# Optimization experiments

Hardware: AMD Instinct MI355X
Metric: run time of the kernel (lower is better)

## Reference

```python
import jax, jax.numpy as jnp
import numpy as np

# GlobalAttention block from GATESynergy: to_dense_batch -> multi-head
# masked self-attention per graph -> scatter back to sparse + residual.
B, NMAX, DIN, DOUT, H = 512, 160, 128, 128, 4
DH = DOUT // H  # 32
COUNTS = np.where(np.arange(B) % 2 == 0, 96, 160)  # nodes per graph, sum=65536
T = int(COUNTS.sum())


def _xavier(key, dout, din):
    lim = np.sqrt(6.0 / (din + dout)).astype(np.float32)
    return jax.random.uniform(key, (dout, din), jnp.float32, -lim, lim)


def setup_inputs() -> dict:
    key = jax.random.key(0)
    ks = jax.random.split(key, 5)
    batch = jnp.asarray(np.repeat(np.arange(B), COUNTS), dtype=jnp.int32)
    x = jax.random.normal(ks[0], (T, DIN), jnp.float32)
    return {
        "x": x,
        "batch": batch,
        "Wq": _xavier(ks[1], DOUT, DIN), "bq": jnp.zeros((DOUT,), jnp.float32),
        "Wk": _xavier(ks[2], DOUT, DIN), "bk": jnp.zeros((DOUT,), jnp.float32),
        "Wv": _xavier(ks[3], DOUT, DIN), "bv": jnp.zeros((DOUT,), jnp.float32),
        "Wo": _xavier(ks[4], DOUT, DOUT), "bo": jnp.zeros((DOUT,), jnp.float32),
    }


def reference(x, batch, Wq, bq, Wk, bk, Wv, bv, Wo, bo):
    n = x.shape[0]
    # --- to_dense_batch: sparse [T, D] -> dense [B, NMAX, D] + mask ---
    counts = jax.ops.segment_sum(jnp.ones(n, jnp.int32), batch, num_segments=B)
    starts = jnp.cumsum(counts) - counts            # first node index per graph
    pos = jnp.arange(n, dtype=jnp.int32) - starts[batch]  # slot within graph
    x_dense = jnp.zeros((B, NMAX, DIN), x.dtype).at[batch, pos].set(x)
    mask = jnp.zeros((B, NMAX), bool).at[batch, pos].set(True)

    def proj(W, b):  # [B,N,DIN] -> [B,H,N,DH]
        return (x_dense @ W.T + b).reshape(B, NMAX, H, DH).transpose(0, 2, 1, 3)

    q, k, v = proj(Wq, bq), proj(Wk, bk), proj(Wv, bv)
    scores = jnp.einsum('bhnd,bhmd->bhnm', q, k) / jnp.sqrt(jnp.asarray(DH, x.dtype))
    scores = jnp.where(mask[:, None, None, :], scores, -jnp.inf)  # mask keys
    attn = jax.nn.softmax(scores, axis=-1)  # dropout p=0.0 -> identity
    out = jnp.einsum('bhnm,bhmd->bnhd', attn, v).reshape(B, NMAX, DOUT)
    out = out @ Wo.T + bo
    out_sparse = out[batch, pos]  # gather valid nodes back to sparse layout
    return out_sparse + x  # residual: in_channels == out_channels
```

## Files before the change

### kernel.cpp

```cpp
#include <hip/hip_runtime.h>

typedef unsigned short u16;
typedef unsigned int u32;
typedef __attribute__((ext_vector_type(8))) short bf16x8;
typedef __attribute__((ext_vector_type(4))) float f32x4;

__device__ __forceinline__ u16 f2bf(float f) {
  u32 u = __builtin_bit_cast(u32, f);
  u += 0x7fffu + ((u >> 16) & 1u);
  return (u16)(u >> 16);
}
__device__ __forceinline__ short f2bs(float f) { return (short)f2bf(f); }

__device__ __forceinline__ bf16x8 cvt8(const float* p) {
  f32x4 a = *reinterpret_cast<const f32x4*>(p);
  f32x4 b = *reinterpret_cast<const f32x4*>(p + 4);
  bf16x8 r;
  r[0] = f2bs(a[0]); r[1] = f2bs(a[1]); r[2] = f2bs(a[2]); r[3] = f2bs(a[3]);
  r[4] = f2bs(b[0]); r[5] = f2bs(b[1]); r[6] = f2bs(b[2]); r[7] = f2bs(b[3]);
  return r;
}
__device__ __forceinline__ bf16x8 lds8(const u16* p) {
  return *reinterpret_cast<const bf16x8*>(p);
}

#define MFMA(a, b, c) __builtin_amdgcn_mfma_f32_16x16x32_bf16((a), (b), (c), 0, 0, 0)

constexpr int DIN = 128, DOUT = 128, DH = 32;
constexpr int T = 65536;
constexpr size_t WFOFF = 0;
constexpr size_t QOFF = 65536;
constexpr size_t KOFF = QOFF + (size_t)4 * T * DH;
constexpr size_t VOFF = KOFF + (size_t)4 * T * DH;
constexpr size_t WS_NEED = (VOFF + (size_t)4 * T * DH) * 2;

__device__ __forceinline__ size_t fragoff(int mat, int ft, int ks) {
  return ((size_t)((mat * 8 + ft) * 4 + ks)) << 9;
}

__global__ void cvtw_kernel(const float* __restrict__ Wq, const float* __restrict__ Wk,
                            const float* __restrict__ Wv, const float* __restrict__ Wo,
                            u16* __restrict__ wf) {
  const int fl = blockIdx.x * 256 + threadIdx.x;
  const int lane = fl & 63, ks = (fl >> 6) & 3, ft = (fl >> 8) & 7, mat = fl >> 11;
  const float* src = mat == 0 ? Wq : mat == 1 ? Wk : mat == 2 ? Wv : Wo;
  const int lr = lane & 15, lg = lane >> 4;
  bf16x8 r = cvt8(src + (ft * 16 + lr) * DIN + ks * 32 + lg * 8);
  *reinterpret_cast<bf16x8*>(wf + (size_t)fl * 8) = r;
}

__global__ __launch_bounds__(256, 2) void qkv_kernel(const float* __restrict__ x,
                                                     const float* __restrict__ bq,
                                                     const float* __restrict__ bk,
                                                     const float* __restrict__ bv,
                                                     u16* __restrict__ ws) {
  const int tid = threadIdx.x;
  const int w = tid >> 6, lane = tid & 63, lg = lane >> 4, lr = lane & 15;
  const size_t rbase = (size_t)blockIdx.x * 128 + w * 32;
  const f32x4 zero = {0.f, 0.f, 0.f, 0.f};
  const u16* wf = ws + WFOFF;
  u16* Q = ws + QOFF;
  u16* K = ws + KOFF;
  u16* V = ws + VOFF;

  bf16x8 xa[2][4];
#pragma unroll
  for (int rt = 0; rt < 2; ++rt)
#pragma unroll
    for (int ks = 0; ks < 4; ++ks)
      xa[rt][ks] = cvt8(x + (rbase + rt * 16 + lr) * DIN + ks * 32 + lg * 8);

#pragma unroll
  for (int ft = 0; ft < 8; ++ft) {
    const int h = ft >> 1, dt = ft & 1;
    bf16x8 wqf[4], wkf[4], wvf[4];
#pragma unroll
    for (int ks = 0; ks < 4; ++ks) {
      wqf[ks] = lds8(wf + fragoff(0, ft, ks) + lane * 8);
      wkf[ks] = lds8(wf + fragoff(1, ft, ks) + lane * 8);
      wvf[ks] = lds8(wf + fragoff(2, ft, ks) + lane * 8);
    }
    f32x4 qacc[2], kacc[2], vacc[2];
#pragma unroll
    for (int rt = 0; rt < 2; ++rt) qacc[rt] = kacc[rt] = vacc[rt] = zero;
#pragma unroll
    for (int rt = 0; rt < 2; ++rt)
#pragma unroll
      for (int ks = 0; ks < 4; ++ks) {
        qacc[rt] = MFMA(xa[rt][ks], wqf[ks], qacc[rt]);
        kacc[rt] = MFMA(xa[rt][ks], wkf[ks], kacc[rt]);
        vacc[rt] = MFMA(wvf[ks], xa[rt][ks], vacc[rt]);
      }
    const float bqv = bq[ft * 16 + lr], bkv = bk[ft * 16 + lr];
    float bvj[4];
#pragma unroll
    for (int j = 0; j < 4; ++j) bvj[j] = bv[ft * 16 + lg * 4 + j];
#pragma unroll
    for (int rt = 0; rt < 2; ++rt) {
      const size_t row0 = rbase + rt * 16;
      const size_t qk_base = (size_t)h * T * DH + (row0 + lg * 4) * DH + dt * 16 + lr;
      const size_t v_base = (size_t)h * T * DH + (((rbase >> 5) + (rt >> 1)) << 10) +
                            (size_t)(dt * 16 + lg * 4) * 32 + (rt & 1) * 16 + lr;
#pragma unroll
      for (int j = 0; j < 4; ++j) {
        Q[qk_base + (size_t)j * DH] = f2bf(qacc[rt][j] + bqv);
        K[qk_base + (size_t)j * DH] = f2bf(kacc[rt][j] + bkv);
        V[v_base + (size_t)j * 32] = f2bf(vacc[rt][j] + bvj[j]);
      }
    }
  }
}

template <int C>
__device__ void attn_wave(const u16* __restrict__ Qh, const u16* __restrict__ Kh,
                          const u16* __restrict__ Vh, int start, int h, int rt,
                          u16 (&strip)[16][168], u16 (&otile)[16][136]) {
  constexpr int NT = C / 16, KB = C / 32;
  const int lane = threadIdx.x & 63, lg = lane >> 4, lr = lane & 15;
  const f32x4 zero = {0.f, 0.f, 0.f, 0.f};
  const int gr = start + rt * 16;

  bf16x8 vb[KB][2];
#pragma unroll
  for (int ks = 0; ks < KB; ++ks)
#pragma unroll
    for (int dt = 0; dt < 2; ++dt)
      vb[ks][dt] = lds8(Vh + (((size_t)(start >> 5) + ks) << 10) +
                        (size_t)(dt * 16 + lr) * 32 + lg * 8);

  const bf16x8 qa = lds8(Qh + (size_t)(gr + lr) * DH + lg * 8);
  f32x4 sacc[NT];
#pragma unroll
  for (int ct = 0; ct < NT; ++ct)
    sacc[ct] = MFMA(qa, lds8(Kh + (size_t)(start + ct * 16 + lr) * DH + lg * 8), zero);

  const float scale = 0.17677669529663687f;
  float m[4], s[4];
#pragma unroll
  for (int j = 0; j < 4; ++j) {
    m[j] = sacc[0][j];
#pragma unroll
    for (int ct = 1; ct < NT; ++ct) m[j] = fmaxf(m[j], sacc[ct][j]);
  }
#pragma unroll
  for (int d = 1; d < 16; d <<= 1) {
#pragma unroll
    for (int j = 0; j < 4; ++j) m[j] = fmaxf(m[j], __shfl_xor(m[j], d, 64));
  }
#pragma unroll
  for (int j = 0; j < 4; ++j) {
    s[j] = 0.f;
#pragma unroll
    for (int ct = 0; ct < NT; ++ct) {
      const float p = __expf((sacc[ct][j] - m[j]) * scale);
      sacc[ct][j] = p;
      s[j] += p;
    }
  }
#pragma unroll
  for (int d = 1; d < 16; d <<= 1) {
#pragma unroll
    for (int j = 0; j < 4; ++j) s[j] += __shfl_xor(s[j], d, 64);
  }
#pragma unroll
  for (int j = 0; j < 4; ++j) {
    const float inv = 1.0f / s[j];
#pragma unroll
    for (int ct = 0; ct < NT; ++ct)
      strip[lg * 4 + j][ct * 16 + lr] = f2bf(sacc[ct][j] * inv);
  }
  asm volatile("s_waitcnt lgkmcnt(0)" ::: "memory");

  f32x4 o0 = zero, o1 = zero;
#pragma unroll
  for (int ks = 0; ks < KB; ++ks) {
    const bf16x8 pa = lds8(&strip[lr][ks * 32 + lg * 8]);
    o0 = MFMA(pa, vb[ks][0], o0);
    o1 = MFMA(pa, vb[ks][1], o1);
  }
#pragma unroll
  for (int j = 0; j < 4; ++j) {
    otile[lg * 4 + j][h * 32 + lr] = f2bf(o0[j]);
    otile[lg * 4 + j][h * 32 + 16 + lr] = f2bf(o1[j]);
  }
}

__global__ __launch_bounds__(256, 3) void attn_kernel(const u16* __restrict__ ws,
                                                      const float* __restrict__ bo,
                                                      const float* __restrict__ x,
                                                      float* __restrict__ out) {
  __shared__ u16 strip[4][16][168];
  __shared__ u16 otile[16][136];
  const int w = threadIdx.x >> 6, lane = threadIdx.x & 63;
  const int lg = lane >> 4, lr = lane & 15;
  const int phys = blockIdx.x;
  const int xcd = phys & 7, idx = phys >> 3;
  const int t = idx & 15;
  const int p = (idx >> 4) * 8 + xcd;
  const int h = w;
  const u16* Qh = ws + QOFF + (size_t)h * T * DH;
  const u16* Kh = ws + KOFF + (size_t)h * T * DH;
  const u16* Vh = ws + VOFF + (size_t)h * T * DH;

  int gr;
  if (t < 6) {
    attn_wave<96>(Qh, Kh, Vh, p * 256, h, t, strip[w], otile);
    gr = p * 256 + t * 16;
  } else {
    attn_wave<160>(Qh, Kh, Vh, p * 256 + 96, h, t - 6, strip[w], otile);
    gr = p * 256 + 96 + (t - 6) * 16;
  }
  __syncthreads();

  const u16* wf = ws + WFOFF;
  const f32x4 zero = {0.f, 0.f, 0.f, 0.f};
  bf16x8 oa[4];
#pragma unroll
  for (int ks = 0; ks < 4; ++ks) oa[ks] = lds8(&otile[lr][ks * 32 + lg * 8]);
  f32x4 acc0 = zero, acc1 = zero;
#pragma unroll
  for (int ks = 0; ks < 4; ++ks) {
    acc0 = MFMA(oa[ks], lds8(wf + fragoff(3, w * 2, ks) + lane * 8), acc0);
    acc1 = MFMA(oa[ks], lds8(wf + fragoff(3, w * 2 + 1, ks) + lane * 8), acc1);
  }
  const int c0 = w * 32 + lr, c1 = w * 32 + 16 + lr;
  const float b0 = bo[c0], b1 = bo[c1];
#pragma unroll
  for (int j = 0; j < 4; ++j) {
    const size_t n = (size_t)gr + lg * 4 + j;
    out[n * DOUT + c0] = acc0[j] + b0 + x[n * DIN + c0];
    out[n * DOUT + c1] = acc1[j] + b1 + x[n * DIN + c1];
  }
}

struct SLds1 {
  u16 k[160][40];
  u16 vt[32][168];
  u16 strip[4][16][168];
};

template <int C>
__device__ void attn1(const float* __restrict__ xg, const float* __restrict__ Wq,
                      const float* __restrict__ bq, const float* __restrict__ Wk,
                      const float* __restrict__ bk, const float* __restrict__ Wv,
                      const float* __restrict__ bv, float* __restrict__ og, int h, SLds1& sm) {
  constexpr int NT = C / 16, KB = C / 32, SLOTS = (NT + 3) / 4;
  const int tid = threadIdx.x;
  const int w = tid >> 6, lane = tid & 63, lg = lane >> 4, lr = lane & 15;
  const f32x4 zero = {0.f, 0.f, 0.f, 0.f};

  for (int t = w; t < 2 * NT; t += 4) {
    const int rt = t >> 1, dt = t & 1;
    f32x4 kacc = zero, vacc = zero;
#pragma unroll
    for (int ks = 0; ks < 4; ++ks) {
      bf16x8 xa = cvt8(xg + (rt * 16 + lr) * DIN + ks * 32 + lg * 8);
      bf16x8 wk = cvt8(Wk + (h * DH + dt * 16 + lr) * DIN + ks * 32 + lg * 8);
      bf16x8 wv = cvt8(Wv + (h * DH + dt * 16 + lr) * DIN + ks * 32 + lg * 8);
      kacc = MFMA(xa, wk, kacc);
      vacc = MFMA(wv, xa, vacc);
    }
    const float kb_ = bk[h * DH + dt * 16 + lr];
#pragma unroll
    for (int j = 0; j < 4; ++j) {
      sm.k[rt * 16 + lg * 4 + j][dt * 16 + lr] = f2bf(kacc[j] + kb_);
      sm.vt[dt * 16 + lg * 4 + j][rt * 16 + lr] = f2bf(vacc[j] + bv[h * DH + dt * 16 + lg * 4 + j]);
    }
  }
  __syncthreads();

#pragma unroll
  for (int sl = 0; sl < SLOTS; ++sl) {
    const int rt = w + sl * 4;
    if (rt < NT) {
#pragma unroll
      for (int dt = 0; dt < 2; ++dt) {
        f32x4 qacc = zero;
#pragma unroll
        for (int ks = 0; ks < 4; ++ks) {
          bf16x8 xa = cvt8(xg + (rt * 16 + lr) * DIN + ks * 32 + lg * 8);
          bf16x8 wq = cvt8(Wq + (h * DH + dt * 16 + lr) * DIN + ks * 32 + lg * 8);
          qacc = MFMA(xa, wq, qacc);
        }
        const float bias = bq[h * DH + dt * 16 + lr];
#pragma unroll
        for (int j = 0; j < 4; ++j)
          sm.strip[w][lg * 4 + j][dt * 16 + lr] = f2bf(qacc[j] + bias);
      }
      asm volatile("s_waitcnt lgkmcnt(0)" ::: "memory");
      const bf16x8 qa = lds8(&sm.strip[w][lr][lg * 8]);
      f32x4 sacc[NT];
#pragma unroll
      for (int ct = 0; ct < NT; ++ct)
        sacc[ct] = MFMA(qa, lds8(&sm.k[ct * 16 + lr][lg * 8]), zero);
      const float scale = 0.17677669529663687f;
      float m[4], s[4];
#pragma unroll
      for (int j = 0; j < 4; ++j) {
        m[j] = sacc[0][j];
#pragma unroll
        for (int ct = 1; ct < NT; ++ct) m[j] = fmaxf(m[j], sacc[ct][j]);
      }
#pragma unroll
      for (int d = 1; d < 16; d <<= 1)
#pragma unroll
        for (int j = 0; j < 4; ++j) m[j] = fmaxf(m[j], __shfl_xor(m[j], d, 64));
#pragma unroll
      for (int j = 0; j < 4; ++j) {
        s[j] = 0.f;
#pragma unroll
        for (int ct = 0; ct < NT; ++ct) {
          const float p = __expf((sacc[ct][j] - m[j]) * scale);
          sacc[ct][j] = p;
          s[j] += p;
        }
      }
#pragma unroll
      for (int d = 1; d < 16; d <<= 1)
#pragma unroll
        for (int j = 0; j < 4; ++j) s[j] += __shfl_xor(s[j], d, 64);
#pragma unroll
      for (int j = 0; j < 4; ++j) {
        const float inv = 1.0f / s[j];
#pragma unroll
        for (int ct = 0; ct < NT; ++ct)
          sm.strip[w][lg * 4 + j][ct * 16 + lr] = f2bf(sacc[ct][j] * inv);
      }
      asm volatile("s_waitcnt lgkmcnt(0)" ::: "memory");
      f32x4 o0 = zero, o1 = zero;
#pragma unroll
      for (int ks = 0; ks < KB; ++ks) {
        const bf16x8 pa = lds8(&sm.strip[w][lr][ks * 32 + lg * 8]);
        o0 = MFMA(pa, lds8(&sm.vt[lr][ks * 32 + lg * 8]), o0);
        o1 = MFMA(pa, lds8(&sm.vt[16 + lr][ks * 32 + lg * 8]), o1);
      }
#pragma unroll
      for (int j = 0; j < 4; ++j) {
        const int n = rt * 16 + lg * 4 + j;
        og[n * DOUT + h * DH + lr] = o0[j];
        og[n * DOUT + h * DH + 16 + lr] = o1[j];
      }
    }
  }
}

__global__ __launch_bounds__(256, 3) void fb_k1(const float* __restrict__ x,
                                                const float* __restrict__ Wq,
                                                const float* __restrict__ bq,
                                                const float* __restrict__ Wk,
                                                const float* __restrict__ bk,
                                                const float* __restrict__ Wv,
                                                const float* __restrict__ bv,
                                                float* __restrict__ O) {
  __shared__ SLds1 sm;
  const int bid = blockIdx.x;
  const int g = bid >> 2, h = bid & 3;
  const int p = g >> 1;
  if (g & 1)
    attn1<160>(x + (size_t)(p * 256 + 96) * DIN, Wq, bq, Wk, bk, Wv, bv,
               O + (size_t)(p * 256 + 96) * DOUT, h, sm);
  else
    attn1<96>(x + (size_t)(p * 256) * DIN, Wq, bq, Wk, bk, Wv, bv, O + (size_t)(p * 256) * DOUT,
              h, sm);
}

__global__ __launch_bounds__(256, 4) void fb_k2(float* __restrict__ io, const float* __restrict__ x,
                                                const float* __restrict__ Wo,
                                                const float* __restrict__ bo) {
  const int tid = threadIdx.x;
  const int w = tid >> 6, lane = tid & 63, lg = lane >> 4, lr = lane & 15;
  const f32x4 zero = {0.f, 0.f, 0.f, 0.f};
  const int rbase = blockIdx.x * 128 + w * 32;
  bf16x8 oa[2][4];
#pragma unroll
  for (int r = 0; r < 2; ++r)
#pragma unroll
    for (int ks = 0; ks < 4; ++ks)
      oa[r][ks] = cvt8(io + (size_t)(rbase + r * 16 + lr) * DOUT + ks * 32 + lg * 8);
  f32x4 acc[2][8];
#pragma unroll
  for (int r = 0; r < 2; ++r)
#pragma unroll
    for (int jt = 0; jt < 8; ++jt) acc[r][jt] = zero;
#pragma unroll
  for (int jt = 0; jt < 8; ++jt)
#pragma unroll
    for (int ks = 0; ks < 4; ++ks) {
      const bf16x8 wb = cvt8(Wo + (size_t)(jt * 16 + lr) * DOUT + ks * 32 + lg * 8);
      acc[0][jt] = MFMA(oa[0][ks], wb, acc[0][jt]);
      acc[1][jt] = MFMA(oa[1][ks], wb, acc[1][jt]);
    }
#pragma unroll
  for (int r = 0; r < 2; ++r)
#pragma unroll
    for (int jt = 0; jt < 8; ++jt) {
      const int c = jt * 16 + lr;
      const float bias = bo[c];
#pragma unroll
      for (int j = 0; j < 4; ++j) {
        const size_t n = (size_t)rbase + r * 16 + lg * 4 + j;
        io[n * DOUT + c] = acc[r][jt][j] + bias + x[n * DIN + c];
      }
    }
}

extern "C" void kernel_launch(void* const* d_in, const int* in_sizes, int n_in,
                              void* d_out, int out_size, void* d_ws, size_t ws_size,
                              hipStream_t stream) {
  const float* x = (const float*)d_in[0];
  const float* Wq = (const float*)d_in[2];
  const float* bq = (const float*)d_in[3];
  const float* Wk = (const float*)d_in[4];
  const float* bk = (const float*)d_in[5];
  const float* Wv = (const float*)d_in[6];
  const float* bv = (const float*)d_in[7];
  const float* Wo = (const float*)d_in[8];
  const float* bo = (const float*)d_in[9];
  float* out = (float*)d_out;

  if (ws_size >= WS_NEED) {
    u16* ws = (u16*)d_ws;
    cvtw_kernel<<<dim3(32), dim3(256), 0, stream>>>(Wq, Wk, Wv, Wo, ws);
    qkv_kernel<<<dim3(512), dim3(256), 0, stream>>>(x, bq, bk, bv, ws);
    attn_kernel<<<dim3(4096), dim3(256), 0, stream>>>(ws, bo, x, out);
  } else {
    fb_k1<<<dim3(2048), dim3(256), 0, stream>>>(x, Wq, bq, Wk, bk, Wv, bv, out);
    fb_k2<<<dim3(512), dim3(256), 0, stream>>>(out, x, Wo, bo);
  }
}
```

Baseline: 59.16 us.

## Process two query row tiles per wave, reusing K/V fragments and halving grid

Each attention block now handles two 16-row query tiles instead of one. K fragments are loaded once into registers and shared across both tiles, V fragments are reused likewise, and the grid is halved. The residual x values are prefetched before the barrier so those loads overlap the sync. This cuts redundant K/V global loads and per-block overhead, but raises register pressure and reduces parallelism (fewer blocks).

```diff
diff --git a/kernel.cpp b/kernel.cpp
--- a/kernel.cpp
+++ b/kernel.cpp
@@ -112,13 +112,15 @@
 }
 
 template <int C>
-__device__ void attn_wave(const u16* __restrict__ Qh, const u16* __restrict__ Kh,
-                          const u16* __restrict__ Vh, int start, int h, int rt,
-                          u16 (&strip)[16][168], u16 (&otile)[16][136]) {
+__device__ void attn_wave2(const u16* __restrict__ Qh, const u16* __restrict__ Kh,
+                           const u16* __restrict__ Vh, const u16* __restrict__ wf,
+                           const float* __restrict__ bo, const float* __restrict__ x,
+                           float* __restrict__ out, int start, int h, int t0,
+                           u16 (&strip)[16][168], u16 (&otile)[2][16][136]) {
   constexpr int NT = C / 16, KB = C / 32;
   const int lane = threadIdx.x & 63, lg = lane >> 4, lr = lane & 15;
   const f32x4 zero = {0.f, 0.f, 0.f, 0.f};
-  const int gr = start + rt * 16;
+  const int w = h;
 
   bf16x8 vb[KB][2];
 #pragma unroll
@@ -127,61 +129,103 @@
     for (int dt = 0; dt < 2; ++dt)
       vb[ks][dt] = lds8(Vh + (((size_t)(start >> 5) + ks) << 10) +
                         (size_t)(dt * 16 + lr) * 32 + lg * 8);
-
-  const bf16x8 qa = lds8(Qh + (size_t)(gr + lr) * DH + lg * 8);
-  f32x4 sacc[NT];
+  bf16x8 kf[NT];
 #pragma unroll
   for (int ct = 0; ct < NT; ++ct)
-    sacc[ct] = MFMA(qa, lds8(Kh + (size_t)(start + ct * 16 + lr) * DH + lg * 8), zero);
-
-  const float scale = 0.17677669529663687f;
-  float m[4], s[4];
-#pragma unroll
-  for (int j = 0; j < 4; ++j) {
-    m[j] = sacc[0][j];
-#pragma unroll
-    for (int ct = 1; ct < NT; ++ct) m[j] = fmaxf(m[j], sacc[ct][j]);
-  }
-#pragma unroll
-  for (int d = 1; d < 16; d <<= 1) {
-#pragma unroll
-    for (int j = 0; j < 4; ++j) m[j] = fmaxf(m[j], __shfl_xor(m[j], d, 64));
-  }
-#pragma unroll
-  for (int j = 0; j < 4; ++j) {
-    s[j] = 0.f;
-#pragma unroll
-    for (int ct = 0; ct < NT; ++ct) {
-      const float p = __expf((sacc[ct][j] - m[j]) * scale);
-      sacc[ct][j] = p;
-      s[j] += p;
-    }
-  }
-#pragma unroll
-  for (int d = 1; d < 16; d <<= 1) {
-#pragma unroll
-    for (int j = 0; j < 4; ++j) s[j] += __shfl_xor(s[j], d, 64);
-  }
-#pragma unroll
-  for (int j = 0; j < 4; ++j) {
-    const float inv = 1.0f / s[j];
-#pragma unroll
-    for (int ct = 0; ct < NT; ++ct)
-      strip[lg * 4 + j][ct * 16 + lr] = f2bf(sacc[ct][j] * inv);
-  }
-  asm volatile("s_waitcnt lgkmcnt(0)" ::: "memory");
-
-  f32x4 o0 = zero, o1 = zero;
-#pragma unroll
-  for (int ks = 0; ks < KB; ++ks) {
-    const bf16x8 pa = lds8(&strip[lr][ks * 32 + lg * 8]);
-    o0 = MFMA(pa, vb[ks][0], o0);
-    o1 = MFMA(pa, vb[ks][1], o1);
-  }
-#pragma unroll
-  for (int j = 0; j < 4; ++j) {
-    otile[lg * 4 + j][h * 32 + lr] = f2bf(o0[j]);
-    otile[lg * 4 + j][h * 32 + 16 + lr] = f2bf(o1[j]);
+    kf[ct] = lds8(Kh + (size_t)(start + ct * 16 + lr) * DH + lg * 8);
+
+#pragma unroll
+  for (int r = 0; r < 2; ++r) {
+    const int gr = start + (t0 + r) * 16;
+    const bf16x8 qa = lds8(Qh + (size_t)(gr + lr) * DH + lg * 8);
+    f32x4 sacc[NT];
+#pragma unroll
+    for (int ct = 0; ct < NT; ++ct) sacc[ct] = MFMA(qa, kf[ct], zero);
+
+    const float scale = 0.17677669529663687f;
+    float m[4], s[4];
+#pragma unroll
+    for (int j = 0; j < 4; ++j) {
+      m[j] = sacc[0][j];
+#pragma unroll
+      for (int ct = 1; ct < NT; ++ct) m[j] = fmaxf(m[j], sacc[ct][j]);
+    }
+#pragma unroll
+    for (int d = 1; d < 16; d <<= 1) {
+#pragma unroll
+      for (int j = 0; j < 4; ++j) m[j] = fmaxf(m[j], __shfl_xor(m[j], d, 64));
+    }
+#pragma unroll
+    for (int j = 0; j < 4; ++j) {
+      s[j] = 0.f;
+#pragma unroll
+      for (int ct = 0; ct < NT; ++ct) {
+        const float p = __expf((sacc[ct][j] - m[j]) * scale);
+        sacc[ct][j] = p;
+        s[j] += p;
+      }
+    }
+#pragma unroll
+    for (int d = 1; d < 16; d <<= 1) {
+#pragma unroll
+      for (int j = 0; j < 4; ++j) s[j] += __shfl_xor(s[j], d, 64);
+    }
+#pragma unroll
+    for (int j = 0; j < 4; ++j) {
+      const float inv = 1.0f / s[j];
+#pragma unroll
+      for (int ct = 0; ct < NT; ++ct)
+        strip[lg * 4 + j][ct * 16 + lr] = f2bf(sacc[ct][j] * inv);
+    }
+    asm volatile("s_waitcnt lgkmcnt(0)" ::: "memory");
+
+    f32x4 o0 = zero, o1 = zero;
+#pragma unroll
+    for (int ks = 0; ks < KB; ++ks) {
+      const bf16x8 pa = lds8(&strip[lr][ks * 32 + lg * 8]);
+      o0 = MFMA(pa, vb[ks][0], o0);
+      o1 = MFMA(pa, vb[ks][1], o1);
+    }
+#pragma unroll
+    for (int j = 0; j < 4; ++j) {
+      otile[r][lg * 4 + j][h * 32 + lr] = f2bf(o0[j]);
+      otile[r][lg * 4 + j][h * 32 + 16 + lr] = f2bf(o1[j]);
+    }
+  }
+
+  const int c0 = w * 32 + lr, c1 = w * 32 + 16 + lr;
+  float xr0[2][4], xr1[2][4];
+#pragma unroll
+  for (int r = 0; r < 2; ++r) {
+    const int gr = start + (t0 + r) * 16;
+#pragma unroll
+    for (int j = 0; j < 4; ++j) {
+      const size_t n = (size_t)gr + lg * 4 + j;
+      xr0[r][j] = x[n * DIN + c0];
+      xr1[r][j] = x[n * DIN + c1];
+    }
+  }
+  __syncthreads();
+
+  const float b0 = bo[c0], b1 = bo[c1];
+#pragma unroll
+  for (int r = 0; r < 2; ++r) {
+    bf16x8 oa[4];
+#pragma unroll
+    for (int ks = 0; ks < 4; ++ks) oa[ks] = lds8(&otile[r][lr][ks * 32 + lg * 8]);
+    f32x4 acc0 = zero, acc1 = zero;
+#pragma unroll
+    for (int ks = 0; ks < 4; ++ks) {
+      acc0 = MFMA(oa[ks], lds8(wf + fragoff(3, w * 2, ks) + lane * 8), acc0);
+      acc1 = MFMA(oa[ks], lds8(wf + fragoff(3, w * 2 + 1, ks) + lane * 8), acc1);
+    }
+    const int gr = start + (t0 + r) * 16;
+#pragma unroll
+    for (int j = 0; j < 4; ++j) {
+      const size_t n = (size_t)gr + lg * 4 + j;
+      out[n * DOUT + c0] = acc0[j] + b0 + xr0[r][j];
+      out[n * DOUT + c1] = acc1[j] + b1 + xr1[r][j];
+    }
   }
 }
 
@@ -190,47 +234,23 @@
                                                       const float* __restrict__ x,
                                                       float* __restrict__ out) {
   __shared__ u16 strip[4][16][168];
-  __shared__ u16 otile[16][136];
-  const int w = threadIdx.x >> 6, lane = threadIdx.x & 63;
-  const int lg = lane >> 4, lr = lane & 15;
+  __shared__ u16 otile[2][16][136];
+  const int w = threadIdx.x >> 6;
   const int phys = blockIdx.x;
   const int xcd = phys & 7, idx = phys >> 3;
-  const int t = idx & 15;
-  const int p = (idx >> 4) * 8 + xcd;
+  const int u = idx & 7;
+  const int p = (idx >> 3) * 8 + xcd;
   const int h = w;
+  const int t0 = u * 2;
   const u16* Qh = ws + QOFF + (size_t)h * T * DH;
   const u16* Kh = ws + KOFF + (size_t)h * T * DH;
   const u16* Vh = ws + VOFF + (size_t)h * T * DH;
-
-  int gr;
-  if (t < 6) {
-    attn_wave<96>(Qh, Kh, Vh, p * 256, h, t, strip[w], otile);
-    gr = p * 256 + t * 16;
-  } else {
-    attn_wave<160>(Qh, Kh, Vh, p * 256 + 96, h, t - 6, strip[w], otile);
-    gr = p * 256 + 96 + (t - 6) * 16;
-  }
-  __syncthreads();
-
   const u16* wf = ws + WFOFF;
-  const f32x4 zero = {0.f, 0.f, 0.f, 0.f};
-  bf16x8 oa[4];
-#pragma unroll
-  for (int ks = 0; ks < 4; ++ks) oa[ks] = lds8(&otile[lr][ks * 32 + lg * 8]);
-  f32x4 acc0 = zero, acc1 = zero;
-#pragma unroll
-  for (int ks = 0; ks < 4; ++ks) {
-    acc0 = MFMA(oa[ks], lds8(wf + fragoff(3, w * 2, ks) + lane * 8), acc0);
-    acc1 = MFMA(oa[ks], lds8(wf + fragoff(3, w * 2 + 1, ks) + lane * 8), acc1);
-  }
-  const int c0 = w * 32 + lr, c1 = w * 32 + 16 + lr;
-  const float b0 = bo[c0], b1 = bo[c1];
-#pragma unroll
-  for (int j = 0; j < 4; ++j) {
-    const size_t n = (size_t)gr + lg * 4 + j;
-    out[n * DOUT + c0] = acc0[j] + b0 + x[n * DIN + c0];
-    out[n * DOUT + c1] = acc1[j] + b1 + x[n * DIN + c1];
-  }
+
+  if (t0 < 6)
+    attn_wave2<96>(Qh, Kh, Vh, wf, bo, x, out, p * 256, h, t0, strip[w], otile);
+  else
+    attn_wave2<160>(Qh, Kh, Vh, wf, bo, x, out, p * 256 + 96, h, t0 - 6, strip[w], otile);
 }
 
 struct SLds1 {
@@ -422,7 +442,7 @@
     u16* ws = (u16*)d_ws;
     cvtw_kernel<<<dim3(32), dim3(256), 0, stream>>>(Wq, Wk, Wv, Wo, ws);
     qkv_kernel<<<dim3(512), dim3(256), 0, stream>>>(x, bq, bk, bv, ws);
-    attn_kernel<<<dim3(4096), dim3(256), 0, stream>>>(ws, bo, x, out);
+    attn_kernel<<<dim3(2048), dim3(256), 0, stream>>>(ws, bo, x, out);
   } else {
     fb_k1<<<dim3(2048), dim3(256), 0, stream>>>(x, Wq, bq, Wk, bk, Wv, bv, out);
     fb_k2<<<dim3(512), dim3(256), 0, stream>>>(out, x, Wo, bo);
```

After: 57.52 us. -2.8%, faster.
